# Kernel tuning notes

Hardware: AMD Instinct MI355X
Metric: run time of the kernel (lower is better)

## Reference

```python
import jax, jax.numpy as jnp
import numpy as np
from jax import lax

B = 256
NUM_CLASSES = 10
IN_CAPS = 32 * 6 * 6  # 1152
IN_DIM = 8
OUT_DIM = 16
NUM_ITERS = 3


def squash(t, axis=-1):
    sq = jnp.sum(t * t, axis=axis, keepdims=True)
    return (sq / (1.0 + sq)) * t / jnp.sqrt(sq)


def conv2d(x, w, b, stride):
    y = lax.conv_general_dilated(x, w, (stride, stride), 'VALID',
                                 dimension_numbers=('NCHW', 'OIHW', 'NCHW'))
    return y + b[None, :, None, None]


def setup_inputs() -> dict:
    key = jax.random.key(0)
    ks = jax.random.split(key, 12)
    f = jnp.float32
    return {
        'x': jax.random.uniform(ks[0], (B, 1, 28, 28), dtype=f),
        'conv1_w': jax.random.normal(ks[1], (256, 1, 9, 9), dtype=f) * 0.05,
        'conv1_b': jnp.zeros((256,), dtype=f),
        'prim_w': jax.random.normal(ks[2], (IN_DIM * 32, 256, 9, 9), dtype=f) * 0.02,
        'prim_b': jnp.zeros((IN_DIM * 32,), dtype=f),
        'route_w': jax.random.normal(ks[3], (NUM_CLASSES, IN_CAPS, IN_DIM, OUT_DIM), dtype=f),
        'dec_w1': jax.random.normal(ks[4], (OUT_DIM * NUM_CLASSES, 512), dtype=f) * 0.05,
        'dec_b1': jnp.zeros((512,), dtype=f),
        'dec_w2': jax.random.normal(ks[5], (512, 1024), dtype=f) * 0.04,
        'dec_b2': jnp.zeros((1024,), dtype=f),
        'dec_w3': jax.random.normal(ks[6], (1024, 28 * 28), dtype=f) * 0.03,
        'dec_b3': jnp.zeros((28 * 28,), dtype=f),
    }


def reference(x, conv1_w, conv1_b, prim_w, prim_b, route_w,
              dec_w1, dec_b1, dec_w2, dec_b2, dec_w3, dec_b3):
    bsz = x.shape[0]
    # conv1 + relu -> [B,256,20,20]
    h = jax.nn.relu(conv2d(x, conv1_w, conv1_b, 1))
    # primary capsules: 8 parallel convs (stacked into one) -> [B, 8*32, 6, 6]
    p = conv2d(h, prim_w, prim_b, 2)
    # each capsule conv flattens to [B, 32*36], concatenated along last dim
    p = p.reshape(bsz, IN_DIM, 32 * 6 * 6).transpose(0, 2, 1)  # [B, 1152, 8]
    u = squash(p, axis=-1)
    # priors: [o, b, i, d_out]
    priors = jnp.einsum('bic,oicd->obid', u, route_w)
    # routing by agreement: softmax over in_capsules (dim i), per original code
    logits = jnp.zeros((NUM_CLASSES, bsz, IN_CAPS, 1), dtype=priors.dtype)
    outputs = None
    for it in range(NUM_ITERS):
        probs = jax.nn.softmax(logits, axis=2)              # [o,b,i,1]
        outputs = squash(jnp.sum(probs * priors, axis=2, keepdims=True))  # [o,b,1,d]
        if it != NUM_ITERS - 1:
            logits = logits + jnp.sum(priors * outputs, axis=-1, keepdims=True)
    vecs = outputs.reshape(NUM_CLASSES, bsz, OUT_DIM).transpose(1, 0, 2)  # [B,10,16]
    classes = jnp.sqrt(jnp.sum(vecs * vecs, axis=-1))
    classes = jax.nn.softmax(classes, axis=1)               # [B,10]
    # y=None path: one-hot of predicted class (non-differentiable mask)
    y = jax.nn.one_hot(jnp.argmax(classes, axis=1), NUM_CLASSES, dtype=vecs.dtype)
    dec_in = (vecs * y[:, :, None]).reshape(bsz, -1)        # [B,160]
    hdec = jax.nn.relu(dec_in @ dec_w1 + dec_b1)
    hdec = jax.nn.relu(hdec @ dec_w2 + dec_b2)
    reconstruction = jax.nn.sigmoid(hdec @ dec_w3 + dec_b3)  # [B,784]
    return classes, reconstruction
```

## Files before the change

### kernel.cpp

```cpp
#include <hip/hip_runtime.h>
#include <hip/hip_bf16.h>
#include <math.h>


typedef __attribute__((ext_vector_type(8))) short bf16x8;
typedef __attribute__((ext_vector_type(4))) float f32x4;

__device__ __forceinline__ void gl16(const void* g, void* l) {
  __builtin_amdgcn_global_load_lds((const __attribute__((address_space(1))) void*)g,
                                   (__attribute__((address_space(3))) void*)l,
                                   16, 0, 0);
}

__global__ __launch_bounds__(256) void k_conv1(const float* __restrict__ x,
                                               const float* __restrict__ w,
                                               const float* __restrict__ bias,
                                               __hip_bfloat16* __restrict__ hT) {
  const int bid = blockIdx.x;
  const int img = bid >> 2, ocq = bid & 3;
  __shared__ float xs[784];
  __shared__ float ws[64 * 81];
  __shared__ __attribute__((aligned(16))) __hip_bfloat16 tile[8 * 1288];
  const int t = threadIdx.x;
  const float4* xg = (const float4*)(x + (size_t)img * 784);
  if (t < 196) ((float4*)xs)[t] = xg[t];
  const float4* wg = (const float4*)(w + (size_t)ocq * 64 * 81);
  for (int i = t; i < 1296; i += 256) ((float4*)ws)[i] = wg[i];
  __syncthreads();
  const int ocl = t & 63, rowg = t >> 6;
  const int oc = ocq * 64 + ocl;
  const int chl = ocl >> 3, icl = ocl & 7;
  const float bv = bias[oc];
  __hip_bfloat16* hb = hT + ((size_t)img * 32 + ocq * 8) * 6560;
#pragma unroll 1
  for (int it = 0; it < 5; it++) {
    const int r = it * 4 + rowg;
    float acc[20];
#pragma unroll
    for (int p = 0; p < 20; p++) acc[p] = bv;
#pragma unroll
    for (int ky = 0; ky < 9; ky++) {
      float xr[28];
      const float* xrow = &xs[(r + ky) * 28];
#pragma unroll
      for (int q = 0; q < 7; q++) ((float4*)xr)[q] = ((const float4*)xrow)[q];
      float wr[9];
#pragma unroll
      for (int i = 0; i < 9; i++) wr[i] = ws[ocl * 81 + ky * 9 + i];
#pragma unroll
      for (int kx = 0; kx < 9; kx++)
#pragma unroll
        for (int p = 0; p < 20; p++)
          acc[p] = fmaf(wr[kx], xr[p + kx], acc[p]);
    }
#pragma unroll
    for (int p = 0; p < 20; p++) {
      const float v = fmaxf(acc[p], 0.f);
      const __hip_bfloat16 hi = __float2bfloat16(v);
      const __hip_bfloat16 lo = __float2bfloat16(v - __bfloat162float(hi));
      tile[chl * 1288 + (p * 8 + rowg * 2) * 8 + icl] = hi;
      tile[chl * 1288 + (p * 8 + rowg * 2 + 1) * 8 + icl] = lo;
    }
    __syncthreads();
#pragma unroll
    for (int q = 0; q < 5; q++) {
      const int idx = q * 256 + t;
      const int c2 = idx / 160, rem = idx - c2 * 160;
      const int xx = rem >> 3, j = rem & 7;
      const float4 vdat = *(const float4*)&tile[c2 * 1288 + rem * 8];
      *(float4*)(hb + (size_t)c2 * 6560 + (size_t)(xx * 41 + it * 8 + j) * 8) = vdat;
    }
    __syncthreads();
  }
}

__global__ __launch_bounds__(256) void k_wrep(const float* __restrict__ pw,
                                              __hip_bfloat16* __restrict__ wGp) {
  const int s = blockIdx.x >> 2, ocq = blockIdx.x & 3;
  const int ch = s / 21, tq = s - ch * 21;
  __hip_bfloat16* outp = wGp + ((size_t)s * 4 + ocq) * 4608;
  const int t = threadIdx.x;
  for (int e = t; e < 2048; e += 256) {
    const int ocl = e >> 5, k = e & 31;
    const int tapl = k >> 3, icl = k & 7;
    const int tap = tq * 4 + tapl, ic = ch * 8 + icl;
    const int oc = ocq * 64 + ocl;
    const float v = (tap < 81) ? pw[((size_t)oc * 256 + ic) * 81 + tap] : 0.f;
    const __hip_bfloat16 hi = __float2bfloat16(v);
    const __hip_bfloat16 lo = __float2bfloat16(v - __bfloat162float(hi));
    outp[ocl * 72 + k] = hi;
    outp[ocl * 72 + 32 + k] = lo;
  }
  for (int e = t; e < 512; e += 256) {
    const int ocl = e >> 3, j = e & 7;
    outp[ocl * 72 + 64 + j] = __float2bfloat16(0.f);
  }
}

__global__ __launch_bounds__(256) void k_rrep(const float* __restrict__ rw,
                                              float* __restrict__ rwT) {
  const int o = blockIdx.x / 18, ig = blockIdx.x % 18;
  __shared__ float tile[64 * 129];
  const int t = threadIdx.x;
  for (int idx = t; idx < 64 * 128; idx += 256) {
    const int i = idx >> 7, cd = idx & 127;
    tile[i * 129 + cd] = rw[((size_t)o * 1152 + ig * 64 + i) * 128 + cd];
  }
  __syncthreads();
  for (int idx = t; idx < 64 * 128; idx += 256) {
    const int cd = idx >> 6, il = idx & 63;
    rwT[((size_t)o * 128 + cd) * 1152 + ig * 64 + il] = tile[il * 129 + cd];
  }
}

#define HT_B 52480
#define PQ_F 2359296
__global__ __launch_bounds__(512) void k_conv2(
    const __hip_bfloat16* __restrict__ hTg,
    const __hip_bfloat16* __restrict__ wGp,
    float* __restrict__ pq, int c0) {
  __shared__ char hT[HT_B];
  const int bid = blockIdx.x;
  int ig, ocq, kq;
  if (gridDim.x == 512) {
    ig = (bid & 7) | (((bid >> 5) & 7) << 3);
    ocq = (bid >> 3) & 3;
    kq = bid >> 8;
  } else {
    ig = bid >> 3;
    ocq = (bid >> 1) & 3;
    kq = bid & 1;
  }
  const int t = threadIdx.x;
  const int w = t >> 6, lane = t & 63;
  const int lquad = lane >> 4, lrow = lane & 15;
  const int mhalf = w >> 2;
  const int nt = mhalf ? 4 : 5;
  const int mtb = mhalf ? 5 : 0;
  const int ocg = ocq * 64 + (w & 3) * 16 + lrow;
  int abase[5];
#pragma unroll
  for (int i = 0; i < 5; i++) {
    int m = (mtb + i) * 16 + lrow;
    if (i >= nt) m = 0;
    const int img = m / 36, px = m - img * 36;
    const int oy = px / 6, ox = px - oy * 6;
    abase[i] = img * 13120 + ox * 1312 + oy * 64;
  }
  f32x4 acc[5];
#pragma unroll
  for (int i = 0; i < 5; i++) acc[i] = (f32x4){0.f, 0.f, 0.f, 0.f};

  const char* hgc = (const char*)hTg;
  const char* wp = (const char*)wGp + ((size_t)(kq * 336) * 4 + ocq) * 4608 +
                   ((w & 3) * 16 + lrow) * 144 + lquad * 16;
  bf16x8 bh = *(const bf16x8*)wp;
  bf16x8 bl = *(const bf16x8*)(wp + 64);
  wp += 18432;
#pragma unroll 1
  for (int chl = 0; chl < 16; chl++) {
    const int ch = kq * 16 + chl;
    const char* hch = hgc + ((size_t)(ig * 128) + ch) * 13120;
#pragma unroll
    for (int rr = 0; rr < 6; rr++) {
      const int idx = t + rr * 512;
      const int j = idx / 820, r = idx - j * 820;
      gl16(hch + (size_t)j * 419840 + r * 16, hT + rr * 8192 + w * 1024);
    }
    if (t < 208) {
      const int idx = 3072 + t;
      const int j = idx / 820, r = idx - j * 820;
      gl16(hch + (size_t)j * 419840 + r * 16, hT + 49152 + w * 1024);
    }
    __syncthreads();
#pragma unroll 1
    for (int tq = 0; tq < 21; tq++) {
      const bf16x8 nh = *(const bf16x8*)wp;
      const bf16x8 nl = *(const bf16x8*)(wp + 64);
      wp += 18432;
      const int tt = tq * 4 + lquad;
      const int ky = tt / 9, kx = tt - ky * 9;
      const int toff = kx * 656 + ky * 32;
      bf16x8 ah[5];
#pragma unroll
      for (int i = 0; i < 5; i++)
        ah[i] = *(const bf16x8*)(hT + abase[i] + toff);
#pragma unroll
      for (int i = 0; i < 5; i++)
        if (i < nt) acc[i] = __builtin_amdgcn_mfma_f32_16x16x32_bf16(ah[i], bh, acc[i], 0, 0, 0);
#pragma unroll
      for (int i = 0; i < 5; i++)
        if (i < nt) acc[i] = __builtin_amdgcn_mfma_f32_16x16x32_bf16(ah[i], bl, acc[i], 0, 0, 0);
      bf16x8 al[5];
#pragma unroll
      for (int i = 0; i < 5; i++)
        al[i] = *(const bf16x8*)(hT + abase[i] + toff + 16);
#pragma unroll
      for (int i = 0; i < 5; i++)
        if (i < nt) acc[i] = __builtin_amdgcn_mfma_f32_16x16x32_bf16(al[i], bh, acc[i], 0, 0, 0);
      bh = nh;
      bl = nl;
    }
    __syncthreads();
  }
  float* pblk = pq + (size_t)kq * PQ_F;
#pragma unroll
  for (int i = 0; i < 5; i++) {
    if (i < nt) {
#pragma unroll
      for (int r = 0; r < 4; r++) {
        const int m = (mtb + i) * 16 + lquad * 4 + r;
        const int img = m / 36, px = m - img * 36;
        pblk[((size_t)(c0 + ig * 4 + img) * 36 + px) * 256 + ocg] = acc[i][r];
      }
    }
  }
}

__global__ __launch_bounds__(256) void k_squash(const float* __restrict__ pq,
                                                const float* __restrict__ bias,
                                                float* __restrict__ u) {
  const int gid = blockIdx.x * 256 + threadIdx.x;
  const int b = gid / 1152, i = gid - b * 1152;
  const int cp = i / 36, px = i - cp * 36;
  const float* pb = pq + ((size_t)b * 36 + px) * 256 + cp;
  float s[8];
#pragma unroll
  for (int d = 0; d < 8; d++)
    s[d] = pb[d * 32] + pb[(size_t)PQ_F + d * 32] + bias[cp + d * 32];
  float sq = 0.f;
#pragma unroll
  for (int d = 0; d < 8; d++) sq = fmaf(s[d], s[d], sq);
  const float scale = sq / ((1.f + sq) * sqrtf(sq));
  float o[8];
#pragma unroll
  for (int d = 0; d < 8; d++) o[d] = s[d] * scale;
  float* ub = u + (size_t)gid * 8;
  ((float4*)ub)[0] = ((float4*)o)[0];
  ((float4*)ub)[1] = ((float4*)o)[1];
}

__device__ __forceinline__ float wsum(float v) {
#pragma unroll
  for (int o = 32; o > 0; o >>= 1) v += __shfl_xor(v, o, 64);
  return v;
}
__device__ __forceinline__ float wmaxr(float v) {
#pragma unroll
  for (int o = 32; o > 0; o >>= 1) v = fmaxf(v, __shfl_xor(v, o, 64));
  return v;
}

__global__ __launch_bounds__(512) void k_route(const float* __restrict__ u,
                                               const float* __restrict__ rwT,
                                               float* __restrict__ vecs) {
  const int o = blockIdx.x >> 8, b = blockIdx.x & 255;
  __shared__ __attribute__((aligned(16))) float pri4[4 * 1152 * 4];
  __shared__ float red[8 * 17];
  __shared__ float redm[8];
  const int t = threadIdx.x;
  const int wave = t >> 6, lane = t & 63;
  const float* ub = u + (size_t)b * 9216;
  const float* rwo = rwT + (size_t)o * 128 * 1152;
#pragma unroll
  for (int ci = 0; ci < 3; ci++) {
    const bool valid = (ci < 2) || (t < 128);
    const int i = valid ? (t + ci * 512) : 0;
    float uv[8];
    *(float4*)&uv[0] = *(const float4*)(ub + i * 8);
    *(float4*)&uv[4] = *(const float4*)(ub + i * 8 + 4);
    float a[16];
#pragma unroll
    for (int d = 0; d < 16; d++) a[d] = 0.f;
#pragma unroll
    for (int c = 0; c < 8; c++) {
      const float* wcol = rwo + (size_t)(c * 16) * 1152 + i;
#pragma unroll
      for (int d = 0; d < 16; d++)
        a[d] = fmaf(uv[c], wcol[(size_t)d * 1152], a[d]);
    }
    if (valid) {
#pragma unroll
      for (int q = 0; q < 4; q++)
        *(float4*)&pri4[(q * 1152 + i) * 4] = *(float4*)&a[q * 4];
    }
  }
  __syncthreads();
  float l[3];
#pragma unroll
  for (int ci = 0; ci < 3; ci++)
    l[ci] = ((ci < 2) || (t < 128)) ? 0.f : -1e30f;
  float v[16];
#pragma unroll 1
  for (int it = 0; it < 3; it++) {
    float m = fmaxf(fmaxf(l[0], l[1]), l[2]);
    m = wmaxr(m);
    if (lane == 0) redm[wave] = m;
    __syncthreads();
    m = redm[0];
#pragma unroll
    for (int wv2 = 1; wv2 < 8; wv2++) m = fmaxf(m, redm[wv2]);
    float Z = 0.f, S[16];
#pragma unroll
    for (int d = 0; d < 16; d++) S[d] = 0.f;
#pragma unroll
    for (int ci = 0; ci < 3; ci++) {
      const bool valid = (ci < 2) || (t < 128);
      const int i = valid ? (t + ci * 512) : 0;
      const float e = expf(l[ci] - m);
      Z += e;
#pragma unroll
      for (int q = 0; q < 4; q++) {
        const float4 p4 = *(const float4*)&pri4[(q * 1152 + i) * 4];
        S[q * 4 + 0] = fmaf(e, p4.x, S[q * 4 + 0]);
        S[q * 4 + 1] = fmaf(e, p4.y, S[q * 4 + 1]);
        S[q * 4 + 2] = fmaf(e, p4.z, S[q * 4 + 2]);
        S[q * 4 + 3] = fmaf(e, p4.w, S[q * 4 + 3]);
      }
    }
    Z = wsum(Z);
#pragma unroll
    for (int d = 0; d < 16; d++) S[d] = wsum(S[d]);
    __syncthreads();
    if (lane == 0) {
      red[wave * 17] = Z;
#pragma unroll
      for (int d = 0; d < 16; d++) red[wave * 17 + 1 + d] = S[d];
    }
    __syncthreads();
    float Zt = 0.f;
#pragma unroll
    for (int wv2 = 0; wv2 < 8; wv2++) Zt += red[wv2 * 17];
    float sv[16], sq = 0.f;
#pragma unroll
    for (int d = 0; d < 16; d++) {
      float sd = 0.f;
#pragma unroll
      for (int wv2 = 0; wv2 < 8; wv2++) sd += red[wv2 * 17 + 1 + d];
      sd /= Zt;
      sv[d] = sd;
      sq = fmaf(sd, sd, sq);
    }
    const float scale = sq / ((1.f + sq) * sqrtf(sq));
#pragma unroll
    for (int d = 0; d < 16; d++) v[d] = scale * sv[d];
    if (it < 2) {
#pragma unroll
      for (int ci = 0; ci < 3; ci++) {
        const bool valid = (ci < 2) || (t < 128);
        const int i = valid ? (t + ci * 512) : 0;
        float dot = 0.f;
#pragma unroll
        for (int q = 0; q < 4; q++) {
          const float4 p4 = *(const float4*)&pri4[(q * 1152 + i) * 4];
          dot = fmaf(p4.x, v[q * 4 + 0], dot);
          dot = fmaf(p4.y, v[q * 4 + 1], dot);
          dot = fmaf(p4.z, v[q * 4 + 2], dot);
          dot = fmaf(p4.w, v[q * 4 + 3], dot);
        }
        l[ci] += dot;
      }
      __syncthreads();
    }
  }
  if (t == 0) {
    float* vb = vecs + ((size_t)b * 10 + o) * 16;
#pragma unroll
    for (int d = 0; d < 16; d++) vb[d] = v[d];
  }
}

__global__ __launch_bounds__(64) void k_cls(const float* __restrict__ vecs,
                                            float* __restrict__ out,
                                            float* __restrict__ selvec,
                                            int* __restrict__ amv) {
  const int b = blockIdx.x * 64 + threadIdx.x;
  const float* vb = vecs + (size_t)b * 160;
  float n[10];
#pragma unroll
  for (int o = 0; o < 10; o++) {
    float sq = 0.f;
#pragma unroll
    for (int d = 0; d < 16; d++) { const float xv = vb[o * 16 + d]; sq = fmaf(xv, xv, sq); }
    n[o] = sqrtf(sq);
  }
  float m = n[0];
#pragma unroll
  for (int o = 1; o < 10; o++) m = fmaxf(m, n[o]);
  float e[10], Z = 0.f;
#pragma unroll
  for (int o = 0; o < 10; o++) { e[o] = expf(n[o] - m); Z += e[o]; }
  const float inv = 1.f / Z;
  float cls[10];
#pragma unroll
  for (int o = 0; o < 10; o++) {
    cls[o] = e[o] * inv;
    out[(size_t)b * 10 + o] = cls[o];
  }
  int am = 0;
  float best = cls[0];
#pragma unroll
  for (int o = 1; o < 10; o++)
    if (cls[o] > best) { best = cls[o]; am = o; }
  amv[b] = am;
#pragma unroll
  for (int d = 0; d < 16; d++) selvec[(size_t)b * 16 + d] = vb[am * 16 + d];
}

__global__ __launch_bounds__(512) void k_dec1(const float* __restrict__ selvec,
                                              const int* __restrict__ amv,
                                              const float* __restrict__ w1,
                                              const float* __restrict__ b1,
                                              float* __restrict__ h1) {
  const int b = blockIdx.x, t = threadIdx.x;
  __shared__ float sv[16];
  __shared__ int ams;
  if (t < 16) sv[t] = selvec[(size_t)b * 16 + t];
  if (t == 0) ams = amv[b];
  __syncthreads();
  const float* wrow = w1 + (size_t)ams * 16 * 512;
  float acc = b1[t];
#pragma unroll
  for (int d = 0; d < 16; d++) acc = fmaf(sv[d], wrow[d * 512 + t], acc);
  h1[(size_t)b * 512 + t] = fmaxf(acc, 0.f);
}

__global__ __launch_bounds__(128) void k_dec2(const float* __restrict__ h1,
                                              const float* __restrict__ w2,
                                              const float* __restrict__ b2,
                                              float* __restrict__ h2) {
  const int nc = blockIdx.x >> 5, bg = blockIdx.x & 31;
  const int t = threadIdx.x;
  const int n = nc * 128 + t;
  const int bs = bg * 8;
  __shared__ float h1s[8 * 512];
  __shared__ float wts[32 * 128];
  {
    const float4* src = (const float4*)(h1 + (size_t)bs * 512);
    for (int i = t; i < 1024; i += 128) ((float4*)h1s)[i] = src[i];
  }
  float acc[8];
  const float bb = b2[n];
#pragma unroll
  for (int j = 0; j < 8; j++) acc[j] = bb;
#pragma unroll 1
  for (int kt = 0; kt < 16; kt++) {
    __syncthreads();
#pragma unroll
    for (int r = 0; r < 32; r++)
      wts[r * 128 + t] = w2[(size_t)(kt * 32 + r) * 1024 + n];
    __syncthreads();
#pragma unroll
    for (int k4 = 0; k4 < 8; k4++) {
      float wq[4];
#pragma unroll
      for (int q = 0; q < 4; q++) wq[q] = wts[(k4 * 4 + q) * 128 + t];
#pragma unroll
      for (int j = 0; j < 8; j++) {
        const float4 hv = *(const float4*)&h1s[j * 512 + kt * 32 + k4 * 4];
        acc[j] = fmaf(hv.x, wq[0], acc[j]);
        acc[j] = fmaf(hv.y, wq[1], acc[j]);
        acc[j] = fmaf(hv.z, wq[2], acc[j]);
        acc[j] = fmaf(hv.w, wq[3], acc[j]);
      }
    }
  }
#pragma unroll
  for (int j = 0; j < 8; j++) h2[(size_t)(bs + j) * 1024 + n] = fmaxf(acc[j], 0.f);
}

__global__ __launch_bounds__(128) void k_dec3(const float* __restrict__ h2,
                                              const float* __restrict__ w3,
                                              const float* __restrict__ b3,
                                              float* __restrict__ out) {
  const int nc = blockIdx.x >> 5, bg = blockIdx.x & 31;
  const int t = threadIdx.x;
  const int bs = bg * 8;
  __shared__ float h2s[8 * 1024];
  __shared__ float wts[32 * 112];
  {
    const float4* src = (const float4*)(h2 + (size_t)bs * 1024);
    for (int i = t; i < 2048; i += 128) ((float4*)h2s)[i] = src[i];
  }
  const int n = nc * 112 + (t < 112 ? t : 0);
  float acc[8];
  const float bb = b3[n];
#pragma unroll
  for (int j = 0; j < 8; j++) acc[j] = bb;
#pragma unroll 1
  for (int kt = 0; kt < 32; kt++) {
    __syncthreads();
#pragma unroll
    for (int r = 0; r < 32; r++)
      if (t < 112) wts[r * 112 + t] = w3[(size_t)(kt * 32 + r) * 784 + n];
    __syncthreads();
    if (t < 112) {
#pragma unroll
      for (int k4 = 0; k4 < 8; k4++) {
        float wq[4];
#pragma unroll
        for (int q = 0; q < 4; q++) wq[q] = wts[(k4 * 4 + q) * 112 + t];
#pragma unroll
        for (int j = 0; j < 8; j++) {
          const float4 hv = *(const float4*)&h2s[j * 1024 + kt * 32 + k4 * 4];
          acc[j] = fmaf(hv.x, wq[0], acc[j]);
          acc[j] = fmaf(hv.y, wq[1], acc[j]);
          acc[j] = fmaf(hv.z, wq[2], acc[j]);
          acc[j] = fmaf(hv.w, wq[3], acc[j]);
        }
      }
    }
  }
  if (t < 112) {
#pragma unroll
    for (int j = 0; j < 8; j++)
      out[(size_t)(bs + j) * 784 + n] = 1.f / (1.f + expf(-acc[j]));
  }
}

extern "C" void kernel_launch(void* const* d_in, const int* in_sizes, int n_in,
                              void* d_out, int out_size, void* d_ws, size_t ws_size,
                              hipStream_t stream) {
  const float* x   = (const float*)d_in[0];
  const float* c1w = (const float*)d_in[1];
  const float* c1b = (const float*)d_in[2];
  const float* pw  = (const float*)d_in[3];
  const float* pb  = (const float*)d_in[4];
  const float* rw  = (const float*)d_in[5];
  const float* w1  = (const float*)d_in[6];
  const float* b1  = (const float*)d_in[7];
  const float* w2  = (const float*)d_in[8];
  const float* b2  = (const float*)d_in[9];
  const float* w3  = (const float*)d_in[10];
  const float* b3  = (const float*)d_in[11];
  float* out = (float*)d_out;
  float* ws = (float*)d_ws;

  const size_t WGP_F = ((size_t)672 * 4 * 4608 + 18432) / 4;
  const size_t U_F = 2359296;
  const size_t RWT_F = 10 * 128 * 1152;
  const size_t SMALL_F = 40960 + 4096 + 256 + 131072 + 262144;
  const size_t fixed_f = WGP_F + 2 * PQ_F + U_F + RWT_F + SMALL_F;
  int chunk = 256;
  while (chunk > 8 && (fixed_f + (size_t)chunk * 104960) * 4 > ws_size) chunk >>= 1;

  __hip_bfloat16* wGp  = (__hip_bfloat16*)ws;
  __hip_bfloat16* hTgc = (__hip_bfloat16*)(ws + WGP_F);
  float* pq   = ws + WGP_F + (size_t)chunk * 104960;
  float* u    = pq + 2 * PQ_F;
  float* rwT  = u + U_F;
  float* vecs = rwT + RWT_F;
  float* sel  = vecs + 40960;
  int*   amv  = (int*)(sel + 4096);
  float* h1   = sel + 4096 + 256;
  float* h2   = h1 + 131072;

  k_wrep<<<dim3(2688), dim3(256), 0, stream>>>(pw, wGp);
  k_rrep<<<dim3(180), dim3(256), 0, stream>>>(rw, rwT);
  for (int c0 = 0; c0 < 256; c0 += chunk) {
    k_conv1<<<dim3(chunk * 4), dim3(256), 0, stream>>>(x + (size_t)c0 * 784, c1w, c1b, hTgc);
    k_conv2<<<dim3((chunk / 4) * 8), dim3(512), 0, stream>>>(hTgc, wGp, pq, c0);
  }
  k_squash<<<dim3(1152), dim3(256), 0, stream>>>(pq, pb, u);
  k_route<<<dim3(2560), dim3(512), 0, stream>>>(u, rwT, vecs);
  k_cls<<<dim3(4), dim3(64), 0, stream>>>(vecs, out, sel, amv);
  k_dec1<<<dim3(256), dim3(512), 0, stream>>>(sel, amv, w1, b1, h1);
  k_dec2<<<dim3(256), dim3(128), 0, stream>>>(h1, w2, b2, h2);
  k_dec3<<<dim3(224), dim3(128), 0, stream>>>(h2, w3, b3, out + 2560);
}
```

Measured before the change: 877.3 us.

## Store conv1 output in parity-split layout to cut LDS bank conflicts in conv2

Conv1 now writes its bf16 hi/lo activations in a layout split by x/y parity and by hi/lo half, padded to 11-element strides, and conv2's LDS addressing and tap offsets are changed to match. The aim is to make the strided stride-2 conv reads from LDS hit different banks, reducing bank conflicts in the MFMA inner loop. This costs a larger per-channel footprint (more LDS per block and more workspace), which may reduce occupancy or the chunk size. Separately, the routing kernel's block-to-(class,batch) mapping is reordered so that neighbouring blocks share batch data.

```diff
diff --git a/kernel.cpp b/kernel.cpp
--- a/kernel.cpp
+++ b/kernel.cpp
@@ -11,6 +11,10 @@
                                    (__attribute__((address_space(3))) void*)l,
                                    16, 0, 0);
 }
+
+#define IC_CHUNKS 891
+#define IC_BYTES  14256
+#define IC_ELEMS  7128
 
 __global__ __launch_bounds__(256) void k_conv1(const float* __restrict__ x,
                                                const float* __restrict__ w,
@@ -31,7 +35,7 @@
   const int oc = ocq * 64 + ocl;
   const int chl = ocl >> 3, icl = ocl & 7;
   const float bv = bias[oc];
-  __hip_bfloat16* hb = hT + ((size_t)img * 32 + ocq * 8) * 6560;
+  __hip_bfloat16* hb = hT + ((size_t)img * 32 + ocq * 8) * IC_ELEMS;
 #pragma unroll 1
   for (int it = 0; it < 5; it++) {
     const int r = it * 4 + rowg;
@@ -67,8 +71,11 @@
       const int idx = q * 256 + t;
       const int c2 = idx / 160, rem = idx - c2 * 160;
       const int xx = rem >> 3, j = rem & 7;
+      const int y = it * 4 + (j >> 1), half = j & 1;
+      const int cc = ((xx & 1) * 2 + (y & 1)) * 222 + half * 111 +
+                     (xx >> 1) * 11 + (y >> 1);
       const float4 vdat = *(const float4*)&tile[c2 * 1288 + rem * 8];
-      *(float4*)(hb + (size_t)c2 * 6560 + (size_t)(xx * 41 + it * 8 + j) * 8) = vdat;
+      *(float4*)(hb + (size_t)c2 * IC_ELEMS + (size_t)cc * 8) = vdat;
     }
     __syncthreads();
   }
@@ -113,7 +120,7 @@
   }
 }
 
-#define HT_B 52480
+#define HT_B 57024
 #define PQ_F 2359296
 __global__ __launch_bounds__(512) void k_conv2(
     const __hip_bfloat16* __restrict__ hTg,
@@ -145,7 +152,7 @@
     if (i >= nt) m = 0;
     const int img = m / 36, px = m - img * 36;
     const int oy = px / 6, ox = px - oy * 6;
-    abase[i] = img * 13120 + ox * 1312 + oy * 64;
+    abase[i] = img * IC_BYTES + (ox * 11 + oy) * 16;
   }
   f32x4 acc[5];
 #pragma unroll
@@ -160,17 +167,17 @@
 #pragma unroll 1
   for (int chl = 0; chl < 16; chl++) {
     const int ch = kq * 16 + chl;
-    const char* hch = hgc + ((size_t)(ig * 128) + ch) * 13120;
+    const char* hch = hgc + ((size_t)(ig * 128) + ch) * IC_BYTES;
 #pragma unroll
     for (int rr = 0; rr < 6; rr++) {
       const int idx = t + rr * 512;
-      const int j = idx / 820, r = idx - j * 820;
-      gl16(hch + (size_t)j * 419840 + r * 16, hT + rr * 8192 + w * 1024);
-    }
-    if (t < 208) {
+      const int j = idx / IC_CHUNKS, r = idx - j * IC_CHUNKS;
+      gl16(hch + (size_t)j * (32 * IC_BYTES) + r * 16, hT + rr * 8192 + w * 1024);
+    }
+    if (t < 492) {
       const int idx = 3072 + t;
-      const int j = idx / 820, r = idx - j * 820;
-      gl16(hch + (size_t)j * 419840 + r * 16, hT + 49152 + w * 1024);
+      const int j = idx / IC_CHUNKS, r = idx - j * IC_CHUNKS;
+      gl16(hch + (size_t)j * (32 * IC_BYTES) + r * 16, hT + 49152 + w * 1024);
     }
     __syncthreads();
 #pragma unroll 1
@@ -180,7 +187,8 @@
       wp += 18432;
       const int tt = tq * 4 + lquad;
       const int ky = tt / 9, kx = tt - ky * 9;
-      const int toff = kx * 656 + ky * 32;
+      const int toff = (((kx & 1) * 2 + (ky & 1)) * 222 +
+                        (kx >> 1) * 11 + (ky >> 1)) * 16;
       bf16x8 ah[5];
 #pragma unroll
       for (int i = 0; i < 5; i++)
@@ -194,7 +202,7 @@
       bf16x8 al[5];
 #pragma unroll
       for (int i = 0; i < 5; i++)
-        al[i] = *(const bf16x8*)(hT + abase[i] + toff + 16);
+        al[i] = *(const bf16x8*)(hT + abase[i] + toff + 111 * 16);
 #pragma unroll
       for (int i = 0; i < 5; i++)
         if (i < nt) acc[i] = __builtin_amdgcn_mfma_f32_16x16x32_bf16(al[i], bh, acc[i], 0, 0, 0);
@@ -254,7 +262,10 @@
 __global__ __launch_bounds__(512) void k_route(const float* __restrict__ u,
                                                const float* __restrict__ rwT,
                                                float* __restrict__ vecs) {
-  const int o = blockIdx.x >> 8, b = blockIdx.x & 255;
+  const int bid = blockIdx.x;
+  int o, b;
+  if (bid < 2048) { o = bid & 7; b = bid >> 3; }
+  else { const int ix = bid - 2048; o = 8 + (ix & 1); b = ix >> 1; }
   __shared__ __attribute__((aligned(16))) float pri4[4 * 1152 * 4];
   __shared__ float red[8 * 17];
   __shared__ float redm[8];
@@ -542,11 +553,11 @@
   const size_t SMALL_F = 40960 + 4096 + 256 + 131072 + 262144;
   const size_t fixed_f = WGP_F + 2 * PQ_F + U_F + RWT_F + SMALL_F;
   int chunk = 256;
-  while (chunk > 8 && (fixed_f + (size_t)chunk * 104960) * 4 > ws_size) chunk >>= 1;
+  while (chunk > 8 && (fixed_f + (size_t)chunk * 114048) * 4 > ws_size) chunk >>= 1;
 
   __hip_bfloat16* wGp  = (__hip_bfloat16*)ws;
   __hip_bfloat16* hTgc = (__hip_bfloat16*)(ws + WGP_F);
-  float* pq   = ws + WGP_F + (size_t)chunk * 104960;
+  float* pq   = ws + WGP_F + (size_t)chunk * 114048;
   float* u    = pq + 2 * PQ_F;
   float* rwT  = u + U_F;
   float* vecs = rwT + RWT_F;
```

Result: slower. 903.7 us (+3.0%).
